# Kernel tuning notes

Measured on AMD Instinct MI355X. Metric: run time of the kernel, lower is better.

The kernel has to match this reference:

```python
import jax, jax.numpy as jnp
import numpy as np


def setup_inputs() -> dict:
    key = jax.random.key(0)
    ks = jax.random.split(key, 6)
    B, Q, K = 4, 512, 1024
    Dq, Dk, Dv, H = 512, 512, 512, 128
    return {
        "queries": jax.random.normal(ks[0], (B, Q, Dq), dtype=jnp.float32),
        "keys": jax.random.normal(ks[1], (B, K, Dk), dtype=jnp.float32),
        "values": jax.random.normal(ks[2], (B, K, Dv), dtype=jnp.float32),
        "W_q": jax.random.normal(ks[3], (Dq, H), dtype=jnp.float32) / np.sqrt(Dq),
        "W_k": jax.random.normal(ks[4], (Dk, H), dtype=jnp.float32) / np.sqrt(Dk),
        "w_v": jax.random.normal(ks[5], (H,), dtype=jnp.float32) / np.sqrt(H),
    }


def reference(queries, keys, values, W_q, W_k, w_v):
    # Additive (Bahdanau) attention.
    q = jnp.einsum("bqd,dh->bqh", queries, W_q)          # [B,Q,H]
    k = jnp.einsum("bkd,dh->bkh", keys, W_k)             # [B,K,H]
    features = jnp.tanh(q[:, :, None, :] + k[:, None, :, :])  # [B,Q,K,H]
    scores = jnp.einsum("bqkh,h->bqk", features, w_v)    # [B,Q,K]
    attn = jax.nn.softmax(scores, axis=-1)               # [B,Q,K]
    return jnp.einsum("bqk,bkv->bqv", attn, values)      # [B,Q,Dv]
```

## Files before the change

### kernel.cpp

```cpp
#include <hip/hip_runtime.h>

#define BB   4
#define QS   512
#define KSZ  1024
#define DD   512
#define HH   128
#define DVV  512
#define KPN  16

typedef unsigned int uint;
typedef unsigned short ushort;
typedef unsigned long long ull;
typedef __attribute__((ext_vector_type(8)))  short short8;
typedef __attribute__((ext_vector_type(16))) float f32x16;
typedef __attribute__((ext_vector_type(2)))  float f32x2;

__device__ __forceinline__ float rcp_fast(float x)  { return __builtin_amdgcn_rcpf(x); }
__device__ __forceinline__ float exp2_fast(float x) { return __builtin_amdgcn_exp2f(x); }
__device__ __forceinline__ f32x2 lo2(float4 v) { return (f32x2){v.x, v.y}; }
__device__ __forceinline__ f32x2 hi2(float4 v) { return (f32x2){v.z, v.w}; }

__device__ __forceinline__ void split1(float v, ushort& h, ushort& l) {
    uint u = __float_as_uint(v);
    h = (ushort)(u >> 16);
    float r = v - __uint_as_float(u & 0xffff0000u);
    l = (ushort)(__float_as_uint(r) >> 16);
}

__device__ __forceinline__ int hperm(int h) {
    return (h & ~3) | ((h & 1) << 1) | ((h >> 1) & 1);
}

#define NSQ  (BB * QS * DD / 4 / 256)
#define NSK  (BB * KSZ * DD / 4 / 256)
#define NWT  128
#define NPJ  192
#define NVT  (BB * (KSZ / 32) * (DVV / 32))

__global__ __launch_bounds__(256) void split_kernel(
    const float* __restrict__ q, const float* __restrict__ k,
    const float* __restrict__ Wq, const float* __restrict__ Wk,
    const float* __restrict__ wv, float* __restrict__ wvp,
    ushort* __restrict__ qh, ushort* __restrict__ ql,
    ushort* __restrict__ kh, ushort* __restrict__ kl,
    ushort* __restrict__ wqh, ushort* __restrict__ wql,
    ushort* __restrict__ wkh, ushort* __restrict__ wkl)
{
    const int id  = blockIdx.x;
    const int tid = threadIdx.x;

    if (id < NSQ + NSK) {
        const float* src; ushort* dh; ushort* dl; size_t i;
        if (id < NSQ) { src = q; dh = qh; dl = ql; i = (size_t)id * 256 + tid; }
        else          { src = k; dh = kh; dl = kl; i = (size_t)(id - NSQ) * 256 + tid; }
        float4 v = ((const float4*)src)[i];
        ushort h0,h1,h2,h3,l0,l1,l2,l3;
        split1(v.x,h0,l0); split1(v.y,h1,l1); split1(v.z,h2,l2); split1(v.w,h3,l3);
        *(ushort4*)&dh[i * 4] = make_ushort4(h0,h1,h2,h3);
        *(ushort4*)&dl[i * 4] = make_ushort4(l0,l1,l2,l3);
        return;
    }
    __shared__ float Ts[32][33];
    int t = id - (NSQ + NSK);
    if (t == 0 && tid < HH) wvp[hperm(tid)] = wv[tid];
    const float* W; ushort* dh; ushort* dl;
    if (t < 64) { W = Wq; dh = wqh; dl = wql; }
    else        { W = Wk; dh = wkh; dl = wkl; t -= 64; }
    const int d0 = (t >> 2) * 32, h0 = (t & 3) * 32;
    {
        const int dd = tid >> 3, c4 = (tid & 7) * 4;
        float4 v = *(const float4*)&W[(size_t)(d0 + dd) * HH + h0 + c4];
        Ts[dd][c4 + 0] = v.x; Ts[dd][c4 + 1] = v.y;
        Ts[dd][c4 + 2] = v.z; Ts[dd][c4 + 3] = v.w;
    }
    __syncthreads();
    {
        const int hh = tid >> 3, d4 = (tid & 7) * 4;
        ushort h[4], l[4];
        #pragma unroll
        for (int i = 0; i < 4; i++) split1(Ts[d4 + i][hh], h[i], l[i]);
        size_t o = (size_t)(h0 + hh) * DD + d0 + d4;
        *(ushort4*)&dh[o] = make_ushort4(h[0], h[1], h[2], h[3]);
        *(ushort4*)&dl[o] = make_ushort4(l[0], l[1], l[2], l[3]);
    }
}

__global__ __launch_bounds__(256) void projvt_kernel(
    const ushort* __restrict__ qh, const ushort* __restrict__ ql,
    const ushort* __restrict__ kh, const ushort* __restrict__ kl,
    const ushort* __restrict__ wqh, const ushort* __restrict__ wql,
    const ushort* __restrict__ wkh, const ushort* __restrict__ wkl,
    const float* __restrict__ val,
    float* __restrict__ eq, float* __restrict__ ek,
    ushort* __restrict__ vhi, ushort* __restrict__ vlo)
{
    const int id  = blockIdx.x;
    const int tid = threadIdx.x;

    if (id >= NPJ) {
        __shared__ float Ts[32][33];
        const int t   = id - NPJ;
        const int b   = t >> 9;
        const int rem = t & 511;
        const int k0  = (rem >> 4) * 32;
        const int n0  = (rem & 15) * 32;
        {
            const int kk = tid >> 3, n4 = (tid & 7) * 4;
            float4 v = *(const float4*)&val[((size_t)b * KSZ + k0 + kk) * DVV + n0 + n4];
            Ts[kk][n4 + 0] = v.x; Ts[kk][n4 + 1] = v.y;
            Ts[kk][n4 + 2] = v.z; Ts[kk][n4 + 3] = v.w;
        }
        __syncthreads();
        {
            const int nn = tid >> 3, k4 = (tid & 7) * 4;
            ushort h[4], l[4];
            #pragma unroll
            for (int i = 0; i < 4; i++) split1(Ts[k4 + i][nn], h[i], l[i]);
            size_t o = ((size_t)b * DVV + n0 + nn) * KSZ + k0 + k4;
            *(ushort4*)&vhi[o] = make_ushort4(h[0], h[1], h[2], h[3]);
            *(ushort4*)&vlo[o] = make_ushort4(l[0], l[1], l[2], l[3]);
        }
        return;
    }

    const int w = tid >> 6, lane = tid & 63;
    const int row = lane & 31, kg = lane >> 5;
    const int gw = id * 4 + w;

    const ushort *pa_h, *pa_l, *pb_h, *pb_l; float* op; int m0, nt;
    if (gw < 256) {
        m0 = (gw >> 2) * 32; nt = gw & 3;
        pa_h = qh; pa_l = ql; pb_h = wqh; pb_l = wql; op = eq;
    } else {
        const int g = gw - 256;
        m0 = (g >> 2) * 32; nt = g & 3;
        pa_h = kh; pa_l = kl; pb_h = wkh; pb_l = wkl; op = ek;
    }

    const ushort* ah_p = pa_h + (size_t)(m0 + row) * DD + kg * 8;
    const ushort* al_p = pa_l + (size_t)(m0 + row) * DD + kg * 8;
    const ushort* bh_p = pb_h + (size_t)(nt * 32 + row) * DD + kg * 8;
    const ushort* bl_p = pb_l + (size_t)(nt * 32 + row) * DD + kg * 8;

    f32x16 acc;
    #pragma unroll
    for (int i = 0; i < 16; i++) acc[i] = 0.f;

    #pragma unroll 8
    for (int ks = 0; ks < DD; ks += 16) {
        short8 ah = *(const short8*)(ah_p + ks);
        short8 al = *(const short8*)(al_p + ks);
        short8 bh = *(const short8*)(bh_p + ks);
        short8 bl = *(const short8*)(bl_p + ks);
        acc = __builtin_amdgcn_mfma_f32_32x32x16_bf16(ah, bh, acc, 0, 0, 0);
        acc = __builtin_amdgcn_mfma_f32_32x32x16_bf16(ah, bl, acc, 0, 0, 0);
        acc = __builtin_amdgcn_mfma_f32_32x32x16_bf16(al, bh, acc, 0, 0, 0);
    }

    const float C2L = 2.8853900817779268f;
    float* ob = op + (size_t)m0 * HH + nt * 32;
    const int prow = hperm(row);
    #pragma unroll
    for (int r = 0; r < 16; r++) {
        const int rb = (r & 3) + 8 * (r >> 2) + 4 * kg;
        ob[(size_t)rb * HH + prow] = fminf(exp2_fast(acc[r] * C2L), 5.0e4f);
    }
}

__global__ __launch_bounds__(256, 4) void spv_kernel(
    const float* __restrict__ eq, const float* __restrict__ ek,
    const float* __restrict__ wvp,
    const ushort* __restrict__ vhi, const ushort* __restrict__ vlo,
    float* __restrict__ opart, float* __restrict__ rsp)
{
    __shared__ float  eqs[32][132];
    __shared__ float  eks[32][132];
    __shared__ ushort PhS[32][36];
    __shared__ ushort PlS[32][36];

    const int id  = blockIdx.x;
    const int kp  = id & 15;
    const int b   = (id >> 4) & 3;
    const int qt  = id >> 6;

    const int tid  = threadIdx.x;
    const int w    = tid >> 6, lane = tid & 63;
    const int tq   = tid >> 4;
    const int tk   = tid & 15;
    const int wn   = w * 128;
    const int arow = lane & 31;
    const int akg  = lane >> 5;

    const float* eqg = eq + ((size_t)b * QS + qt * 32) * HH;
    #pragma unroll
    for (int i = 0; i < 4; i++) {
        int f = tid + i * 256;
        *(float4*)&eqs[f >> 5][(f & 31) * 4] =
            *(const float4*)&eqg[(size_t)(f >> 5) * HH + (f & 31) * 4];
    }
    const float* ekg = ek + ((size_t)b * KSZ + kp * 64) * HH;
    #pragma unroll
    for (int i = 0; i < 4; i++) {
        int f = tid + i * 256;
        *(float4*)&eks[f >> 5][(f & 31) * 4] =
            *(const float4*)&ekg[(size_t)(f >> 5) * HH + (f & 31) * 4];
    }
    __syncthreads();

    f32x16 acc[4];
    #pragma unroll
    for (int n = 0; n < 4; n++) {
        #pragma unroll
        for (int i = 0; i < 16; i++) acc[n][i] = 0.f;
    }
    float rowacc0 = 0.f, rowacc1 = 0.f;

    const size_t vrow0 = ((size_t)b * DVV + wn + arow) * KSZ + kp * 64 + akg * 8;
    const ushort* vhb = vhi + vrow0;
    const ushort* vlb = vlo + vrow0;

    const f32x2 one2 = {1.0f, 1.0f};

#define SGROUP(eq4, ek4, sacc) { \
    f32x2 u02 = __builtin_elementwise_fma(lo2(eq4), lo2(ek4), one2); \
    f32x2 u13 = __builtin_elementwise_fma(hi2(eq4), hi2(ek4), one2); \
    f32x2 p_  = u02 * u13; \
    f32x2 n_  = __builtin_elementwise_fma(wA, u13, wB * u02); \
    float N_  = fmaf(n_.x, p_.y, n_.y * p_.x); \
    sacc = fmaf(N_, rcp_fast(p_.x * p_.y), sacc); }

#define HITER(h) { \
    float4 wp4 = *(const float4*)&wvp[h]; \
    f32x2 wA = lo2(wp4), wB = hi2(wp4); \
    float4 eqa = *(const float4*)&eqs[tq][h]; \
    float4 eqb = *(const float4*)&eqs[tq + 16][h]; \
    float4 eka = *(const float4*)&eks[tk][h]; \
    float4 ekb = *(const float4*)&eks[tk + 16][h]; \
    SGROUP(eqa, eka, s00); SGROUP(eqa, ekb, s01); \
    SGROUP(eqb, eka, s10); SGROUP(eqb, ekb, s11); }

    #pragma unroll
    for (int s = 0; s < 2; s++) {
        float s00 = 0.f, s01 = 0.f, s10 = 0.f, s11 = 0.f;
        #pragma unroll 4
        for (int h = 0; h < HH; h += 4) HITER(h);
        {
            const float CN = -2.8853900817779268f;
            float p00 = exp2_fast(s00 * CN);
            float p01v = exp2_fast(s01 * CN);
            float p10 = exp2_fast(s10 * CN);
            float p11 = exp2_fast(s11 * CN);
            ushort hh, ll;
            split1(p00,  hh, ll); PhS[tq][tk]           = hh; PlS[tq][tk]           = ll;
            split1(p01v, hh, ll); PhS[tq][tk + 16]      = hh; PlS[tq][tk + 16]      = ll;
            split1(p10,  hh, ll); PhS[tq + 16][tk]      = hh; PlS[tq + 16][tk]      = ll;
            split1(p11,  hh, ll); PhS[tq + 16][tk + 16] = hh; PlS[tq + 16][tk + 16] = ll;
            rowacc0 += p00 + p01v;
            rowacc1 += p10 + p11;
        }
        __syncthreads();

        if (s == 0) {
            #pragma unroll
            for (int i = 0; i < 4; i++) {
                int f = tid + i * 256;
                *(float4*)&eks[f >> 5][(f & 31) * 4] =
                    *(const float4*)&ekg[(size_t)(32 + (f >> 5)) * HH + (f & 31) * 4];
            }
        }

        short8 ah0, al0, ah1, al1;
        { const ull* p = (const ull*)&PhS[arow][akg * 8];
          ((ull*)&ah0)[0] = p[0]; ((ull*)&ah0)[1] = p[1]; }
        { const ull* p = (const ull*)&PlS[arow][akg * 8];
          ((ull*)&al0)[0] = p[0]; ((ull*)&al0)[1] = p[1]; }
        { const ull* p = (const ull*)&PhS[arow][16 + akg * 8];
          ((ull*)&ah1)[0] = p[0]; ((ull*)&ah1)[1] = p[1]; }
        { const ull* p = (const ull*)&PlS[arow][16 + akg * 8];
          ((ull*)&al1)[0] = p[0]; ((ull*)&al1)[1] = p[1]; }
        #pragma unroll
        for (int nb = 0; nb < 4; nb++) {
            const size_t o = (size_t)nb * 32 * KSZ + (size_t)s * 32;
            short8 vh0 = *(const short8*)(vhb + o);
            short8 vl0 = *(const short8*)(vlb + o);
            short8 vh1 = *(const short8*)(vhb + o + 16);
            short8 vl1 = *(const short8*)(vlb + o + 16);
            acc[nb] = __builtin_amdgcn_mfma_f32_32x32x16_bf16(ah0, vh0, acc[nb], 0, 0, 0);
            acc[nb] = __builtin_amdgcn_mfma_f32_32x32x16_bf16(ah0, vl0, acc[nb], 0, 0, 0);
            acc[nb] = __builtin_amdgcn_mfma_f32_32x32x16_bf16(al0, vh0, acc[nb], 0, 0, 0);
            acc[nb] = __builtin_amdgcn_mfma_f32_32x32x16_bf16(ah1, vh1, acc[nb], 0, 0, 0);
            acc[nb] = __builtin_amdgcn_mfma_f32_32x32x16_bf16(ah1, vl1, acc[nb], 0, 0, 0);
            acc[nb] = __builtin_amdgcn_mfma_f32_32x32x16_bf16(al1, vh1, acc[nb], 0, 0, 0);
        }
        __syncthreads();
    }
#undef SGROUP
#undef HITER

    #pragma unroll
    for (int m = 8; m; m >>= 1) {
        rowacc0 += __shfl_xor(rowacc0, m);
        rowacc1 += __shfl_xor(rowacc1, m);
    }
    if (tk == 0) {
        rsp[((size_t)b * QS + qt * 32 + tq) * KPN + kp]      = rowacc0;
        rsp[((size_t)b * QS + qt * 32 + tq + 16) * KPN + kp] = rowacc1;
    }

    float* ob = opart + (((size_t)kp * BB + b) * QS + qt * 32) * DVV + wn;
    #pragma unroll
    for (int nb = 0; nb < 4; nb++) {
        #pragma unroll
        for (int r = 0; r < 16; r++) {
            const int rb = (r & 3) + 8 * (r >> 2) + 4 * akg;
            ob[(size_t)rb * DVV + nb * 32 + arow] = acc[nb][r];
        }
    }
}

__global__ __launch_bounds__(256) void norm_kernel(
    const float* __restrict__ opart, const float* __restrict__ rsp,
    float* __restrict__ outp)
{
    const int i  = blockIdx.x * 256 + threadIdx.x;
    const int n4 = (i & 127) * 4;
    const int q  = (i >> 7) & (QS - 1);
    const int b  = i >> 16;

    const float* rp = rsp + ((size_t)b * QS + q) * KPN;
    float s = 0.f;
    #pragma unroll
    for (int j = 0; j < KPN / 4; j++) {
        float4 r = *(const float4*)(rp + j * 4);
        s += r.x + r.y + r.z + r.w;
    }
    float inv = rcp_fast(s);

    float ox = 0.f, oy = 0.f, oz = 0.f, ow = 0.f;
    #pragma unroll
    for (int kp = 0; kp < KPN; kp++) {
        float4 v = *(const float4*)&opart[(((size_t)kp * BB + b) * QS + q) * DVV + n4];
        ox += v.x; oy += v.y; oz += v.z; ow += v.w;
    }
    float4 res = make_float4(ox * inv, oy * inv, oz * inv, ow * inv);
    *(float4*)&outp[((size_t)b * QS + q) * DVV + n4] = res;
}

extern "C" void kernel_launch(void* const* d_in, const int* in_sizes, int n_in,
                              void* d_out, int out_size, void* d_ws, size_t ws_size,
                              hipStream_t stream)
{
    const float* queries = (const float*)d_in[0];
    const float* keys    = (const float*)d_in[1];
    const float* values  = (const float*)d_in[2];
    const float* Wq      = (const float*)d_in[3];
    const float* Wk      = (const float*)d_in[4];
    const float* wv      = (const float*)d_in[5];
    float* out = (float*)d_out;

    float*  eq    = (float*)d_ws;
    float*  ek    = eq  + (size_t)BB * QS * HH;
    float*  rsp   = ek  + (size_t)BB * KSZ * HH;
    float*  wvp   = rsp + (size_t)BB * QS * KPN;
    float*  opart = wvp + 256;
    ushort* vhi = (ushort*)(opart + (size_t)KPN * BB * QS * DVV);
    ushort* vlo = vhi + (size_t)BB * KSZ * DVV;
    ushort* qh  = vlo + (size_t)BB * KSZ * DVV;
    ushort* ql  = qh  + (size_t)BB * QS * DD;
    ushort* kh  = ql  + (size_t)BB * QS * DD;
    ushort* kl  = kh  + (size_t)BB * KSZ * DD;
    ushort* wqh = kl  + (size_t)BB * KSZ * DD;
    ushort* wql = wqh + (size_t)HH * DD;
    ushort* wkh = wql + (size_t)HH * DD;
    ushort* wkl = wkh + (size_t)HH * DD;

    split_kernel<<<dim3(NSQ + NSK + NWT), 256, 0, stream>>>(
        queries, keys, Wq, Wk, wv, wvp, qh, ql, kh, kl, wqh, wql, wkh, wkl);

    projvt_kernel<<<dim3(NPJ + NVT), 256, 0, stream>>>(
        qh, ql, kh, kl, wqh, wql, wkh, wkl, values, eq, ek, vhi, vlo);

    spv_kernel<<<dim3(1024), 256, 0, stream>>>(eq, ek, wvp, vhi, vlo, opart, rsp);

    norm_kernel<<<dim3(1024), 256, 0, stream>>>(opart, rsp, out);
}
```

Before: 150.8 us.

## Enlarge spv tile to 64 queries with 4x4 register blocking and shared V loads

The score/PV kernel now processes 64 queries by 64 keys per block instead of 32 by 64. Each thread computes a 4x4 tile of additive-attention scores, so every shared-memory load of a query or key row feeds more arithmetic. Each V fragment loaded from global memory now feeds MFMAs for two 32-row query halves, roughly halving V traffic. The P tiles reuse the key shared-memory buffer. The grid is halved to 512 blocks and the launch bound drops to 2 blocks per CU, which trades occupancy and latency hiding for more register reuse.

Result: faster. 147.4 us (-2.2%).

```diff
diff --git a/kernel.cpp b/kernel.cpp
--- a/kernel.cpp
+++ b/kernel.cpp
@@ -167,19 +167,19 @@
     }
 }
 
-__global__ __launch_bounds__(256, 4) void spv_kernel(
+__global__ __launch_bounds__(256, 2) void spv_kernel(
     const float* __restrict__ eq, const float* __restrict__ ek,
     const float* __restrict__ wvp,
     const ushort* __restrict__ vhi, const ushort* __restrict__ vlo,
     float* __restrict__ opart, float* __restrict__ rsp)
 {
-    __shared__ float  eqs[32][132];
-    __shared__ float  eks[32][132];
-    __shared__ ushort PhS[32][36];
-    __shared__ ushort PlS[32][36];
+    __shared__ float eqs[64][132];
+    __shared__ float eks[64][132];
+    ushort (*PhS)[68] = (ushort (*)[68])&eks[0][0];
+    ushort (*PlS)[68] = (ushort (*)[68])((ushort*)&eks[0][0] + 64 * 68);
 
     const int id  = blockIdx.x;
-    const int kp  = id & 15;
+    const int kp  = ((id >> 3) & 1) * 8 + (id & 7);
     const int b   = (id >> 4) & 3;
     const int qt  = id >> 6;
 
@@ -191,33 +191,21 @@
     const int arow = lane & 31;
     const int akg  = lane >> 5;
 
-    const float* eqg = eq + ((size_t)b * QS + qt * 32) * HH;
-    #pragma unroll
-    for (int i = 0; i < 4; i++) {
+    const float* eqg = eq + ((size_t)b * QS + qt * 64) * HH;
+    const float* ekg = ek + ((size_t)b * KSZ + kp * 64) * HH;
+    #pragma unroll
+    for (int i = 0; i < 8; i++) {
         int f = tid + i * 256;
         *(float4*)&eqs[f >> 5][(f & 31) * 4] =
             *(const float4*)&eqg[(size_t)(f >> 5) * HH + (f & 31) * 4];
     }
-    const float* ekg = ek + ((size_t)b * KSZ + kp * 64) * HH;
-    #pragma unroll
-    for (int i = 0; i < 4; i++) {
+    #pragma unroll
+    for (int i = 0; i < 8; i++) {
         int f = tid + i * 256;
         *(float4*)&eks[f >> 5][(f & 31) * 4] =
             *(const float4*)&ekg[(size_t)(f >> 5) * HH + (f & 31) * 4];
     }
     __syncthreads();
-
-    f32x16 acc[4];
-    #pragma unroll
-    for (int n = 0; n < 4; n++) {
-        #pragma unroll
-        for (int i = 0; i < 16; i++) acc[n][i] = 0.f;
-    }
-    float rowacc0 = 0.f, rowacc1 = 0.f;
-
-    const size_t vrow0 = ((size_t)b * DVV + wn + arow) * KSZ + kp * 64 + akg * 8;
-    const ushort* vhb = vhi + vrow0;
-    const ushort* vlb = vlo + vrow0;
 
     const f32x2 one2 = {1.0f, 1.0f};
 
@@ -229,91 +217,113 @@
     float N_  = fmaf(n_.x, p_.y, n_.y * p_.x); \
     sacc = fmaf(N_, rcp_fast(p_.x * p_.y), sacc); }
 
-#define HITER(h) { \
-    float4 wp4 = *(const float4*)&wvp[h]; \
-    f32x2 wA = lo2(wp4), wB = hi2(wp4); \
-    float4 eqa = *(const float4*)&eqs[tq][h]; \
-    float4 eqb = *(const float4*)&eqs[tq + 16][h]; \
-    float4 eka = *(const float4*)&eks[tk][h]; \
-    float4 ekb = *(const float4*)&eks[tk + 16][h]; \
-    SGROUP(eqa, eka, s00); SGROUP(eqa, ekb, s01); \
-    SGROUP(eqb, eka, s10); SGROUP(eqb, ekb, s11); }
-
-    #pragma unroll
-    for (int s = 0; s < 2; s++) {
-        float s00 = 0.f, s01 = 0.f, s10 = 0.f, s11 = 0.f;
-        #pragma unroll 4
-        for (int h = 0; h < HH; h += 4) HITER(h);
-        {
-            const float CN = -2.8853900817779268f;
-            float p00 = exp2_fast(s00 * CN);
-            float p01v = exp2_fast(s01 * CN);
-            float p10 = exp2_fast(s10 * CN);
-            float p11 = exp2_fast(s11 * CN);
-            ushort hh, ll;
-            split1(p00,  hh, ll); PhS[tq][tk]           = hh; PlS[tq][tk]           = ll;
-            split1(p01v, hh, ll); PhS[tq][tk + 16]      = hh; PlS[tq][tk + 16]      = ll;
-            split1(p10,  hh, ll); PhS[tq + 16][tk]      = hh; PlS[tq + 16][tk]      = ll;
-            split1(p11,  hh, ll); PhS[tq + 16][tk + 16] = hh; PlS[tq + 16][tk + 16] = ll;
-            rowacc0 += p00 + p01v;
-            rowacc1 += p10 + p11;
-        }
-        __syncthreads();
-
-        if (s == 0) {
-            #pragma unroll
-            for (int i = 0; i < 4; i++) {
-                int f = tid + i * 256;
-                *(float4*)&eks[f >> 5][(f & 31) * 4] =
-                    *(const float4*)&ekg[(size_t)(32 + (f >> 5)) * HH + (f & 31) * 4];
+    float s[4][4];
+    #pragma unroll
+    for (int a = 0; a < 4; a++)
+        #pragma unroll
+        for (int c = 0; c < 4; c++) s[a][c] = 0.f;
+
+    #pragma unroll 4
+    for (int h = 0; h < HH; h += 4) {
+        float4 wp4 = *(const float4*)&wvp[h];
+        f32x2 wA = lo2(wp4), wB = hi2(wp4);
+        float4 eq4[4], ek4[4];
+        #pragma unroll
+        for (int a = 0; a < 4; a++) eq4[a] = *(const float4*)&eqs[tq + 16 * a][h];
+        #pragma unroll
+        for (int c = 0; c < 4; c++) ek4[c] = *(const float4*)&eks[tk + 16 * c][h];
+        #pragma unroll
+        for (int a = 0; a < 4; a++) {
+            #pragma unroll
+            for (int c = 0; c < 4; c++) SGROUP(eq4[a], ek4[c], s[a][c]);
+        }
+    }
+#undef SGROUP
+
+    const float CN = -2.8853900817779268f;
+    float pv[4][4];
+    ushort phv[4][4], plv[4][4];
+    float rowacc[4] = {0.f, 0.f, 0.f, 0.f};
+    #pragma unroll
+    for (int a = 0; a < 4; a++) {
+        #pragma unroll
+        for (int c = 0; c < 4; c++) {
+            pv[a][c] = exp2_fast(s[a][c] * CN);
+            split1(pv[a][c], phv[a][c], plv[a][c]);
+            rowacc[a] += pv[a][c];
+        }
+    }
+
+    __syncthreads();
+
+    #pragma unroll
+    for (int a = 0; a < 4; a++) {
+        #pragma unroll
+        for (int c = 0; c < 4; c++) {
+            PhS[tq + 16 * a][tk + 16 * c] = phv[a][c];
+            PlS[tq + 16 * a][tk + 16 * c] = plv[a][c];
+        }
+    }
+
+    #pragma unroll
+    for (int m = 8; m; m >>= 1) {
+        #pragma unroll
+        for (int a = 0; a < 4; a++) rowacc[a] += __shfl_xor(rowacc[a], m);
+    }
+    if (tk == 0) {
+        #pragma unroll
+        for (int a = 0; a < 4; a++)
+            rsp[((size_t)b * QS + qt * 64 + tq + 16 * a) * KPN + kp] = rowacc[a];
+    }
+
+    __syncthreads();
+
+    f32x16 acc[2][4];
+    #pragma unroll
+    for (int hlf = 0; hlf < 2; hlf++)
+        #pragma unroll
+        for (int nb = 0; nb < 4; nb++)
+            #pragma unroll
+            for (int i = 0; i < 16; i++) acc[hlf][nb][i] = 0.f;
+
+    const size_t vrow0 = ((size_t)b * DVV + wn + arow) * KSZ + kp * 64 + akg * 8;
+    const ushort* vhb = vhi + vrow0;
+    const ushort* vlb = vlo + vrow0;
+
+    #pragma unroll
+    for (int kb = 0; kb < 4; kb++) {
+        short8 ah[2], al[2];
+        #pragma unroll
+        for (int hlf = 0; hlf < 2; hlf++) {
+            { const ull* p = (const ull*)&PhS[hlf * 32 + arow][kb * 16 + akg * 8];
+              ((ull*)&ah[hlf])[0] = p[0]; ((ull*)&ah[hlf])[1] = p[1]; }
+            { const ull* p = (const ull*)&PlS[hlf * 32 + arow][kb * 16 + akg * 8];
+              ((ull*)&al[hlf])[0] = p[0]; ((ull*)&al[hlf])[1] = p[1]; }
+        }
+        #pragma unroll
+        for (int nb = 0; nb < 4; nb++) {
+            const size_t o = (size_t)nb * 32 * KSZ + kb * 16;
+            short8 vh = *(const short8*)(vhb + o);
+            short8 vl = *(const short8*)(vlb + o);
+            #pragma unroll
+            for (int hlf = 0; hlf < 2; hlf++) {
+                acc[hlf][nb] = __builtin_amdgcn_mfma_f32_32x32x16_bf16(ah[hlf], vh, acc[hlf][nb], 0, 0, 0);
+                acc[hlf][nb] = __builtin_amdgcn_mfma_f32_32x32x16_bf16(ah[hlf], vl, acc[hlf][nb], 0, 0, 0);
+                acc[hlf][nb] = __builtin_amdgcn_mfma_f32_32x32x16_bf16(al[hlf], vh, acc[hlf][nb], 0, 0, 0);
             }
         }
-
-        short8 ah0, al0, ah1, al1;
-        { const ull* p = (const ull*)&PhS[arow][akg * 8];
-          ((ull*)&ah0)[0] = p[0]; ((ull*)&ah0)[1] = p[1]; }
-        { const ull* p = (const ull*)&PlS[arow][akg * 8];
-          ((ull*)&al0)[0] = p[0]; ((ull*)&al0)[1] = p[1]; }
-        { const ull* p = (const ull*)&PhS[arow][16 + akg * 8];
-          ((ull*)&ah1)[0] = p[0]; ((ull*)&ah1)[1] = p[1]; }
-        { const ull* p = (const ull*)&PlS[arow][16 + akg * 8];
-          ((ull*)&al1)[0] = p[0]; ((ull*)&al1)[1] = p[1]; }
+    }
+
+    #pragma unroll
+    for (int hlf = 0; hlf < 2; hlf++) {
+        float* ob = opart + (((size_t)kp * BB + b) * QS + qt * 64 + hlf * 32) * DVV + wn;
         #pragma unroll
         for (int nb = 0; nb < 4; nb++) {
-            const size_t o = (size_t)nb * 32 * KSZ + (size_t)s * 32;
-            short8 vh0 = *(const short8*)(vhb + o);
-            short8 vl0 = *(const short8*)(vlb + o);
-            short8 vh1 = *(const short8*)(vhb + o + 16);
-            short8 vl1 = *(const short8*)(vlb + o + 16);
-            acc[nb] = __builtin_amdgcn_mfma_f32_32x32x16_bf16(ah0, vh0, acc[nb], 0, 0, 0);
-            acc[nb] = __builtin_amdgcn_mfma_f32_32x32x16_bf16(ah0, vl0, acc[nb], 0, 0, 0);
-            acc[nb] = __builtin_amdgcn_mfma_f32_32x32x16_bf16(al0, vh0, acc[nb], 0, 0, 0);
-            acc[nb] = __builtin_amdgcn_mfma_f32_32x32x16_bf16(ah1, vh1, acc[nb], 0, 0, 0);
-            acc[nb] = __builtin_amdgcn_mfma_f32_32x32x16_bf16(ah1, vl1, acc[nb], 0, 0, 0);
-            acc[nb] = __builtin_amdgcn_mfma_f32_32x32x16_bf16(al1, vh1, acc[nb], 0, 0, 0);
-        }
-        __syncthreads();
-    }
-#undef SGROUP
-#undef HITER
-
-    #pragma unroll
-    for (int m = 8; m; m >>= 1) {
-        rowacc0 += __shfl_xor(rowacc0, m);
-        rowacc1 += __shfl_xor(rowacc1, m);
-    }
-    if (tk == 0) {
-        rsp[((size_t)b * QS + qt * 32 + tq) * KPN + kp]      = rowacc0;
-        rsp[((size_t)b * QS + qt * 32 + tq + 16) * KPN + kp] = rowacc1;
-    }
-
-    float* ob = opart + (((size_t)kp * BB + b) * QS + qt * 32) * DVV + wn;
-    #pragma unroll
-    for (int nb = 0; nb < 4; nb++) {
-        #pragma unroll
-        for (int r = 0; r < 16; r++) {
-            const int rb = (r & 3) + 8 * (r >> 2) + 4 * akg;
-            ob[(size_t)rb * DVV + nb * 32 + arow] = acc[nb][r];
+            #pragma unroll
+            for (int r = 0; r < 16; r++) {
+                const int rb = (r & 3) + 8 * (r >> 2) + 4 * akg;
+                ob[(size_t)rb * DVV + nb * 32 + arow] = acc[hlf][nb][r];
+            }
         }
     }
 }
@@ -380,7 +390,7 @@
     projvt_kernel<<<dim3(NPJ + NVT), 256, 0, stream>>>(
         qh, ql, kh, kl, wqh, wql, wkh, wkl, values, eq, ek, vhi, vlo);
 
-    spv_kernel<<<dim3(1024), 256, 0, stream>>>(eq, ek, wvp, vhi, vlo, opart, rsp);
+    spv_kernel<<<dim3(512), 256, 0, stream>>>(eq, ek, wvp, vhi, vlo, opart, rsp);
 
     norm_kernel<<<dim3(1024), 256, 0, stream>>>(opart, rsp, out);
 }
```
